# Performance work log

Measured on AMD Instinct MI355X. Metric: run time of the kernel, lower is better.

The kernel has to match this reference:

```python
import jax, jax.numpy as jnp
import numpy as np


def setup_inputs() -> dict:
    key = jax.random.key(0)
    ks = jax.random.split(key, 6)
    B, E, N, F = 512, 4, 256, 64
    node = jax.random.normal(ks[0], (B, N, F), dtype=jnp.float32)
    adj = jax.random.uniform(ks[1], (B, E, N, N), dtype=jnp.float32)
    s = 1.0 / np.sqrt(F)
    W_edge = jax.random.uniform(ks[2], (E, F, F), dtype=jnp.float32, minval=-s, maxval=s)
    b_edge = jax.random.uniform(ks[3], (E, F), dtype=jnp.float32, minval=-s, maxval=s)
    W_add = jax.random.uniform(ks[4], (F, F), dtype=jnp.float32, minval=-s, maxval=s)
    b_add = jax.random.uniform(ks[5], (F,), dtype=jnp.float32, minval=-s, maxval=s)
    return {"node": node, "adj": adj, "W_edge": W_edge, "b_edge": b_edge,
            "W_add": W_add, "b_add": b_add}


def reference(node, adj, W_edge, b_edge, W_add, b_add):
    # per-edge-type linear: [B,N,F_in] x [E,F_in,F_out] -> [B,E,N,F_out]
    hidden = jnp.einsum('bnf,efg->beng', node, W_edge) + b_edge[None, :, None, :]
    # adjacency-weighted aggregation per edge type: [B,E,N,N] @ [B,E,N,F_out]
    msg = jnp.einsum('benm,bemg->beng', adj, hidden)
    # sum over edge types + residual linear (dropout=0, activation=None)
    out = jnp.sum(msg, axis=1) + node @ W_add + b_add
    return out
```

## Files before the change

kernel.cpp:

```cpp
#include <hip/hip_runtime.h>

typedef __attribute__((ext_vector_type(8))) short short8;
typedef __attribute__((ext_vector_type(4))) float f32x4;

#define MFMA16(a, b, c) __builtin_amdgcn_mfma_f32_16x16x32_bf16((a), (b), (c), 0, 0, 0)

static __device__ inline short f2bf(float x) {
    union { float f; unsigned u; } v;
    v.f = x;
    unsigned r = v.u + 0x7fffu + ((v.u >> 16) & 1u);
    return (short)(r >> 16);
}
static __device__ inline short4 f2bf4(float4 v) {
    short4 s;
    s.x = f2bf(v.x); s.y = f2bf(v.y); s.z = f2bf(v.z); s.w = f2bf(v.w);
    return s;
}

__global__ __launch_bounds__(256, 2) void gconv_kernel(
    const float* __restrict__ node,
    const float* __restrict__ adj,
    const float* __restrict__ W_edge,
    const float* __restrict__ b_edge,
    const float* __restrict__ W_add,
    const float* __restrict__ b_add,
    float* __restrict__ out)
{
    constexpr int E = 4;

    __shared__ short adjL[256][72];
    __shared__ short hiddenT[64][264];
    __shared__ short wT[64][72];
    const int b    = blockIdx.x;
    const int t    = threadIdx.x;
    const int lane = t & 63;
    const int w    = t >> 6;
    const int col  = lane & 15;
    const int kq   = lane >> 4;

    const float* nodeB = node + (size_t)b * (256 * 64);
    short8 anode[4][2];
    #pragma unroll
    for (int rt = 0; rt < 4; ++rt)
        #pragma unroll
        for (int h = 0; h < 2; ++h) {
            const float* p = nodeB + (64 * w + 16 * rt + col) * 64 + 32 * h + 8 * kq;
            float4 v0 = *(const float4*)p;
            float4 v1 = *(const float4*)(p + 4);
            short8 a;
            a[0] = f2bf(v0.x); a[1] = f2bf(v0.y); a[2] = f2bf(v0.z); a[3] = f2bf(v0.w);
            a[4] = f2bf(v1.x); a[5] = f2bf(v1.y); a[6] = f2bf(v1.z); a[7] = f2bf(v1.w);
            anode[rt][h] = a;
        }

    #pragma unroll
    for (int i = 0; i < 16; ++i) {
        int idx = i * 256 + t;
        wT[idx & 63][idx >> 6] = f2bf(W_add[idx]);
    }
    __syncthreads();

    f32x4 acc[4][4];
    {
        const f32x4 zf = {0.f, 0.f, 0.f, 0.f};
        #pragma unroll
        for (int rt = 0; rt < 4; ++rt)
            #pragma unroll
            for (int ct = 0; ct < 4; ++ct)
                acc[rt][ct] = zf;
        #pragma unroll
        for (int h = 0; h < 2; ++h) {
            short8 bfr[4];
            #pragma unroll
            for (int ct = 0; ct < 4; ++ct)
                bfr[ct] = *(const short8*)&wT[16 * ct + col][32 * h + 8 * kq];
            #pragma unroll
            for (int rt = 0; rt < 4; ++rt)
                #pragma unroll
                for (int ct = 0; ct < 4; ++ct)
                    acc[rt][ct] = MFMA16(anode[rt][h], bfr[ct], acc[rt][ct]);
        }
    }
    __syncthreads();

    for (int e = 0; e < E; ++e) {
        const float* We = W_edge + e * (64 * 64);
        #pragma unroll
        for (int i = 0; i < 16; ++i) {
            int idx = i * 256 + t;
            wT[idx & 63][idx >> 6] = f2bf(We[idx]);
        }
        __syncthreads();

        #pragma unroll
        for (int rt = 0; rt < 4; ++rt) {
            #pragma unroll
            for (int ct = 0; ct < 4; ++ct) {
                short8 b0 = *(const short8*)&wT[16 * ct + col][8 * kq];
                short8 b1 = *(const short8*)&wT[16 * ct + col][32 + 8 * kq];
                f32x4 h = {0.f, 0.f, 0.f, 0.f};
                h = MFMA16(anode[rt][0], b0, h);
                h = MFMA16(anode[rt][1], b1, h);
                float bias = b_edge[e * 64 + 16 * ct + col];
                short4 s;
                s.x = f2bf(h.x + bias); s.y = f2bf(h.y + bias);
                s.z = f2bf(h.z + bias); s.w = f2bf(h.w + bias);
                *(short4*)&hiddenT[16 * ct + col][64 * w + 16 * rt + 4 * kq] = s;
            }
        }
        __syncthreads();

        const float* adjE = adj + ((size_t)(b * 4 + e)) * (256 * 256);
        for (int kt = 0; kt < 4; ++kt) {
            {
                const int c4  = t & 15;
                const int r0  = t >> 4;
                const float* base = adjE + kt * 64 + c4 * 4;
                #pragma unroll
                for (int i = 0; i < 16; ++i) {
                    int row = i * 16 + r0;
                    float4 v = *(const float4*)(base + row * 256);
                    *(short4*)&adjL[row][c4 * 4] = f2bf4(v);
                }
            }
            __syncthreads();

            #pragma unroll
            for (int ks2 = 0; ks2 < 2; ++ks2) {
                short8 afrag[4], bfrag[4];
                #pragma unroll
                for (int rt = 0; rt < 4; ++rt)
                    afrag[rt] = *(const short8*)&adjL[64 * w + 16 * rt + col][32 * ks2 + 8 * kq];
                #pragma unroll
                for (int ct = 0; ct < 4; ++ct)
                    bfrag[ct] = *(const short8*)&hiddenT[16 * ct + col][kt * 64 + 32 * ks2 + 8 * kq];
                #pragma unroll
                for (int rt = 0; rt < 4; ++rt)
                    #pragma unroll
                    for (int ct = 0; ct < 4; ++ct)
                        acc[rt][ct] = MFMA16(afrag[rt], bfrag[ct], acc[rt][ct]);
            }
            __syncthreads();
        }
    }

    float* outB = out + (size_t)b * (256 * 64);
    #pragma unroll
    for (int ct = 0; ct < 4; ++ct) {
        float bias = b_add[16 * ct + col];
        #pragma unroll
        for (int rt = 0; rt < 4; ++rt) {
            int row = 64 * w + 16 * rt + 4 * kq;
            #pragma unroll
            for (int r = 0; r < 4; ++r)
                outB[(size_t)(row + r) * 64 + 16 * ct + col] = acc[rt][ct][r] + bias;
        }
    }
}

extern "C" void kernel_launch(void* const* d_in, const int* in_sizes, int n_in,
                              void* d_out, int out_size, void* d_ws, size_t ws_size,
                              hipStream_t stream) {
    const float* node   = (const float*)d_in[0];
    const float* adj    = (const float*)d_in[1];
    const float* W_edge = (const float*)d_in[2];
    const float* b_edge = (const float*)d_in[3];
    const float* W_add  = (const float*)d_in[4];
    const float* b_add  = (const float*)d_in[5];
    float* out = (float*)d_out;

    gconv_kernel<<<dim3(512), dim3(256), 0, stream>>>(
        node, adj, W_edge, b_edge, W_add, b_add, out);
}
```

Measured before the change: 714.0 us.

## Tile adjacency by full row strips and prefetch next tile into registers

The adjacency matrix is now staged as 64 full rows (all 256 columns) per step instead of 64-column slabs of all rows, and the node-row mapping per wave is remapped to match. The next 64x256 tile is loaded into registers before the MFMA loop for the current tile runs, so global load latency overlaps compute. Each load is fully contiguous, which should coalesce better. The cost is 64 extra VGPRs for the prefetch buffer, which may strain occupancy at two blocks per CU.

```diff
diff --git a/kernel.cpp b/kernel.cpp
--- a/kernel.cpp
+++ b/kernel.cpp
@@ -26,9 +26,7 @@
     const float* __restrict__ b_add,
     float* __restrict__ out)
 {
-    constexpr int E = 4;
-
-    __shared__ short adjL[256][72];
+    __shared__ short adjL[64][264];
     __shared__ short hiddenT[64][264];
     __shared__ short wT[64][72];
     const int b    = blockIdx.x;
@@ -39,19 +37,29 @@
     const int kq   = lane >> 4;
 
     const float* nodeB = node + (size_t)b * (256 * 64);
+    const float* adjB  = adj  + (size_t)b * (4 * 256 * 256);
+
     short8 anode[4][2];
     #pragma unroll
-    for (int rt = 0; rt < 4; ++rt)
+    for (int st = 0; st < 4; ++st)
         #pragma unroll
         for (int h = 0; h < 2; ++h) {
-            const float* p = nodeB + (64 * w + 16 * rt + col) * 64 + 32 * h + 8 * kq;
+            const float* p = nodeB + (st * 64 + 16 * w + col) * 64 + 32 * h + 8 * kq;
             float4 v0 = *(const float4*)p;
             float4 v1 = *(const float4*)(p + 4);
             short8 a;
             a[0] = f2bf(v0.x); a[1] = f2bf(v0.y); a[2] = f2bf(v0.z); a[3] = f2bf(v0.w);
             a[4] = f2bf(v1.x); a[5] = f2bf(v1.y); a[6] = f2bf(v1.z); a[7] = f2bf(v1.w);
-            anode[rt][h] = a;
+            anode[st][h] = a;
         }
+
+    float4 v[16];
+    {
+        const float* s0 = adjB + t * 4;
+        #pragma unroll
+        for (int i = 0; i < 16; ++i)
+            v[i] = *(const float4*)(s0 + i * 1024);
+    }
 
     #pragma unroll
     for (int i = 0; i < 16; ++i) {
@@ -64,10 +72,10 @@
     {
         const f32x4 zf = {0.f, 0.f, 0.f, 0.f};
         #pragma unroll
-        for (int rt = 0; rt < 4; ++rt)
+        for (int st = 0; st < 4; ++st)
             #pragma unroll
             for (int ct = 0; ct < 4; ++ct)
-                acc[rt][ct] = zf;
+                acc[st][ct] = zf;
         #pragma unroll
         for (int h = 0; h < 2; ++h) {
             short8 bfr[4];
@@ -75,70 +83,67 @@
             for (int ct = 0; ct < 4; ++ct)
                 bfr[ct] = *(const short8*)&wT[16 * ct + col][32 * h + 8 * kq];
             #pragma unroll
-            for (int rt = 0; rt < 4; ++rt)
+            for (int st = 0; st < 4; ++st)
                 #pragma unroll
                 for (int ct = 0; ct < 4; ++ct)
-                    acc[rt][ct] = MFMA16(anode[rt][h], bfr[ct], acc[rt][ct]);
+                    acc[st][ct] = MFMA16(anode[st][h], bfr[ct], acc[st][ct]);
         }
     }
     __syncthreads();
 
-    for (int e = 0; e < E; ++e) {
+    for (int e = 0; e < 4; ++e) {
         const float* We = W_edge + e * (64 * 64);
         #pragma unroll
         for (int i = 0; i < 16; ++i) {
             int idx = i * 256 + t;
             wT[idx & 63][idx >> 6] = f2bf(We[idx]);
         }
+        float bedge[4];
+        #pragma unroll
+        for (int ct = 0; ct < 4; ++ct)
+            bedge[ct] = b_edge[e * 64 + 16 * ct + col];
         __syncthreads();
 
         #pragma unroll
-        for (int rt = 0; rt < 4; ++rt) {
+        for (int ct = 0; ct < 4; ++ct) {
+            short8 b0 = *(const short8*)&wT[16 * ct + col][8 * kq];
+            short8 b1 = *(const short8*)&wT[16 * ct + col][32 + 8 * kq];
             #pragma unroll
-            for (int ct = 0; ct < 4; ++ct) {
-                short8 b0 = *(const short8*)&wT[16 * ct + col][8 * kq];
-                short8 b1 = *(const short8*)&wT[16 * ct + col][32 + 8 * kq];
+            for (int st = 0; st < 4; ++st) {
                 f32x4 h = {0.f, 0.f, 0.f, 0.f};
-                h = MFMA16(anode[rt][0], b0, h);
-                h = MFMA16(anode[rt][1], b1, h);
-                float bias = b_edge[e * 64 + 16 * ct + col];
+                h = MFMA16(anode[st][0], b0, h);
+                h = MFMA16(anode[st][1], b1, h);
                 short4 s;
-                s.x = f2bf(h.x + bias); s.y = f2bf(h.y + bias);
-                s.z = f2bf(h.z + bias); s.w = f2bf(h.w + bias);
-                *(short4*)&hiddenT[16 * ct + col][64 * w + 16 * rt + 4 * kq] = s;
+                s.x = f2bf(h[0] + bedge[ct]); s.y = f2bf(h[1] + bedge[ct]);
+                s.z = f2bf(h[2] + bedge[ct]); s.w = f2bf(h[3] + bedge[ct]);
+                *(short4*)&hiddenT[16 * ct + col][st * 64 + 16 * w + 4 * kq] = s;
             }
         }
         __syncthreads();
 
-        const float* adjE = adj + ((size_t)(b * 4 + e)) * (256 * 256);
-        for (int kt = 0; kt < 4; ++kt) {
-            {
-                const int c4  = t & 15;
-                const int r0  = t >> 4;
-                const float* base = adjE + kt * 64 + c4 * 4;
+        #pragma unroll
+        for (int mt = 0; mt < 4; ++mt) {
+            #pragma unroll
+            for (int i = 0; i < 16; ++i)
+                *(short4*)&adjL[4 * i + w][4 * lane] = f2bf4(v[i]);
+
+            int p = e * 4 + mt;
+            if (p < 15) {
+                const float* s0 = adjB + (size_t)(p + 1) * 16384 + t * 4;
                 #pragma unroll
-                for (int i = 0; i < 16; ++i) {
-                    int row = i * 16 + r0;
-                    float4 v = *(const float4*)(base + row * 256);
-                    *(short4*)&adjL[row][c4 * 4] = f2bf4(v);
-                }
+                for (int i = 0; i < 16; ++i)
+                    v[i] = *(const float4*)(s0 + i * 1024);
             }
             __syncthreads();
 
             #pragma unroll
-            for (int ks2 = 0; ks2 < 2; ++ks2) {
-                short8 afrag[4], bfrag[4];
+            for (int ks = 0; ks < 8; ++ks) {
+                short8 af = *(const short8*)&adjL[16 * w + col][32 * ks + 8 * kq];
                 #pragma unroll
-                for (int rt = 0; rt < 4; ++rt)
-                    afrag[rt] = *(const short8*)&adjL[64 * w + 16 * rt + col][32 * ks2 + 8 * kq];
-                #pragma unroll
-                for (int ct = 0; ct < 4; ++ct)
-                    bfrag[ct] = *(const short8*)&hiddenT[16 * ct + col][kt * 64 + 32 * ks2 + 8 * kq];
-                #pragma unroll
-                for (int rt = 0; rt < 4; ++rt)
-                    #pragma unroll
-                    for (int ct = 0; ct < 4; ++ct)
-                        acc[rt][ct] = MFMA16(afrag[rt], bfrag[ct], acc[rt][ct]);
+                for (int ct = 0; ct < 4; ++ct) {
+                    short8 bf = *(const short8*)&hiddenT[16 * ct + col][32 * ks + 8 * kq];
+                    acc[mt][ct] = MFMA16(af, bf, acc[mt][ct]);
+                }
             }
             __syncthreads();
         }
@@ -149,11 +154,11 @@
     for (int ct = 0; ct < 4; ++ct) {
         float bias = b_add[16 * ct + col];
         #pragma unroll
-        for (int rt = 0; rt < 4; ++rt) {
-            int row = 64 * w + 16 * rt + 4 * kq;
+        for (int st = 0; st < 4; ++st) {
+            int row = st * 64 + 16 * w + 4 * kq;
             #pragma unroll
             for (int r = 0; r < 4; ++r)
-                outB[(size_t)(row + r) * 64 + 16 * ct + col] = acc[rt][ct][r] + bias;
+                outB[(size_t)(row + r) * 64 + 16 * ct + col] = acc[st][ct][r] + bias;
         }
     }
 }
```

New measurement: 710.7 us. No clear change (-0.5%).
